# Kernel tuning notes

Measured on AMD Instinct MI355X. Metric: run time of the kernel, lower is better.

Reference implementation:

```python
import jax, jax.numpy as jnp
import numpy as np

N = 100000        # nodes
E = 1600000       # edges (avg degree 16)
F_IN = 128        # num_node_features
H = 64            # hidden_channels
F_EDGE = 8        # num_edge_features (output dim per edge)


def setup_inputs() -> dict:
    key = jax.random.key(0)
    ks = jax.random.split(key, 9)
    x = jax.random.normal(ks[0], (N, F_IN), dtype=jnp.float32)
    edge_index = jax.random.randint(ks[1], (2, E), 0, N, dtype=jnp.int32)
    s = 0.05
    W1 = jax.random.normal(ks[2], (F_IN, H), jnp.float32) * s
    b1 = jnp.zeros((H,), jnp.float32)
    W2 = jax.random.normal(ks[3], (H, H), jnp.float32) * s
    b2 = jnp.zeros((H,), jnp.float32)
    Wl = jax.random.normal(ks[4], (2 * H, F_EDGE), jnp.float32) * s
    bl = jnp.zeros((F_EDGE,), jnp.float32)
    return {"x": x, "edge_index": edge_index,
            "W1": W1, "b1": b1, "W2": W2, "b2": b2, "Wl": Wl, "bl": bl}


def gcn_conv(x, W, b, row, col, n):
    # GCNConv: h = D^{-1/2} (A + I) D^{-1/2} (x W) + b
    h = x @ W
    sl = jnp.arange(n, dtype=row.dtype)          # self-loops
    r = jnp.concatenate([row, sl])
    c = jnp.concatenate([col, sl])
    ones = jnp.ones(r.shape[0], dtype=h.dtype)
    deg = jax.ops.segment_sum(ones, c, num_segments=n)      # in-degree incl. self-loop
    dinv = jax.lax.rsqrt(jnp.maximum(deg, 1e-12))
    norm = dinv[r] * dinv[c]                                 # symmetric normalization
    agg = jax.ops.segment_sum(norm[:, None] * h[r], c, num_segments=n)
    return agg + b


def reference(x, edge_index, W1, b1, W2, b2, Wl, bl):
    row, col = edge_index[0], edge_index[1]
    h = jax.nn.relu(gcn_conv(x, W1, b1, row, col, N))
    # dropout p=0.5 is identity at inference (training=False)
    h = jax.nn.relu(gcn_conv(h, W2, b2, row, col, N))
    x_i = h[row]                                  # [E, H]
    x_j = h[col]                                  # [E, H]
    return jnp.concatenate([x_i, x_j], axis=-1) @ Wl + bl   # [E, F_EDGE]
```

## Files before the change

### kernel.cpp

```cpp
#include <hip/hip_runtime.h>
#include <hip/hip_bf16.h>

static constexpr int NN  = 100000;
static constexpr int NE  = 1600000;
static constexpr int FIN = 128;
static constexpr int HD  = 64;

static constexpr int NB    = 256;
static constexpr int NPB   = 392;
static constexpr int EPB   = NE / NB;
static constexpr unsigned long long DIV392_MAGIC = 43826197ULL;

static constexpr int NSL = 4;

static constexpr int AGN  = 64;
static constexpr int ACAP = 1536;

typedef __attribute__((ext_vector_type(8))) short bf16x8;
typedef __attribute__((ext_vector_type(4))) float f32x4;

__device__ __forceinline__ float bf2f(unsigned short u) {
    return __uint_as_float(((unsigned int)u) << 16);
}
__device__ __forceinline__ unsigned short f2bf(float f) {
    __hip_bfloat16 hb = __float2bfloat16(f);
    return *(unsigned short*)&hb;
}
__device__ __forceinline__ int bucket_of(int c) {
    return (int)(((unsigned long long)(unsigned int)c * DIV392_MAGIC) >> 34);
}

__device__ __forceinline__ float load_in(const void* p, size_t i, int isbf) {
    return isbf ? bf2f(((const unsigned short*)p)[i]) : ((const float*)p)[i];
}

__global__ __launch_bounds__(256) void k_hist(const int* __restrict__ col, int* __restrict__ hist,
                                              const unsigned short* __restrict__ xu,
                                              int* __restrict__ flag) {
    __shared__ int h[4][NB];
    int t = threadIdx.x, w = t >> 6;
#pragma unroll
    for (int r = 0; r < 4; ++r) h[r][t] = 0;
    __syncthreads();
    int base = blockIdx.x * EPB;
    for (int e = base + t; e < base + EPB; e += 256)
        atomicAdd(&h[w][bucket_of(col[e])], 1);
    __syncthreads();
    hist[t * NB + blockIdx.x] = h[0][t] + h[1][t] + h[2][t] + h[3][t];
    if (blockIdx.x == 0) {
        __syncthreads();
        int cnt = 0;
        for (int k = t; k < 4096; k += 256) {
            unsigned short u = xu[2 * k];
            int ex = (u >> 7) & 0xFF;
            cnt += (ex >= 110 && ex <= 135) ? 1 : 0;
        }
        h[0][t] = cnt;
        __syncthreads();
        for (int off = 128; off > 0; off >>= 1) {
            if (t < off) h[0][t] += h[0][t + off];
            __syncthreads();
        }
        if (t == 0) flag[0] = (h[0][0] >= 2048) ? 1 : 0;
    }
}

__global__ __launch_bounds__(256) void k_gscan1(int* __restrict__ a, int* __restrict__ bsums) {
    __shared__ int sd[256];
    int t = threadIdx.x;
    int base = blockIdx.x * 1024 + t * 4;
    int v0 = a[base], v1 = a[base + 1], v2 = a[base + 2], v3 = a[base + 3];
    int tsum = v0 + v1 + v2 + v3;
    sd[t] = tsum;
    __syncthreads();
    for (int off = 1; off < 256; off <<= 1) {
        int tmp = (t >= off) ? sd[t - off] : 0;
        __syncthreads();
        sd[t] += tmp;
        __syncthreads();
    }
    int run = sd[t] - tsum;
    a[base] = run; run += v0;
    a[base + 1] = run; run += v1;
    a[base + 2] = run; run += v2;
    a[base + 3] = run;
    if (t == 255) bsums[blockIdx.x] = sd[t];
}

__device__ __forceinline__ void scan_bsums(const int* __restrict__ bsumsRaw, int* sb) {
    int t = threadIdx.x;
    int myv = 0;
    if (t < 64) { myv = bsumsRaw[t]; sb[t] = myv; }
    __syncthreads();
    for (int off = 1; off < 64; off <<= 1) {
        int v = (t < 64 && t >= off) ? sb[t - off] : 0;
        __syncthreads();
        if (t < 64) sb[t] += v;
        __syncthreads();
    }
    if (t < 64) sb[t] -= myv;
    __syncthreads();
}

__global__ __launch_bounds__(256) void k_binfill(const int* __restrict__ row, const int* __restrict__ col,
                                                 const int* __restrict__ histS,
                                                 const int* __restrict__ bsumsRaw,
                                                 int* __restrict__ csr_tmp) {
    __shared__ int cur[NB];
    __shared__ int sb[64];
    int t = threadIdx.x;
    scan_bsums(bsumsRaw, sb);
    cur[t] = histS[t * NB + blockIdx.x] + sb[t >> 2];
    __syncthreads();
    int base = blockIdx.x * EPB;
    for (int e = base + t; e < base + EPB; e += 256) {
        int r = row[e], c = col[e];
        int b = bucket_of(c);
        int p = atomicAdd(&cur[b], 1);
        csr_tmp[p] = r | ((c - b * NPB) << 17);
    }
}

__global__ __launch_bounds__(256) void k_bsort(const int* __restrict__ csr_tmp,
                                               const int* __restrict__ histS,
                                               const int* __restrict__ bsumsRaw,
                                               int* __restrict__ csr_src,
                                               int* __restrict__ start,
                                               float* __restrict__ dinv) {
    __shared__ int cnt[512];
    __shared__ int cur[512];
    __shared__ int sb[64];
    int t = threadIdx.x;
    int k = blockIdx.x;
    cnt[t] = 0; cnt[t + 256] = 0;
    scan_bsums(bsumsRaw, sb);
    int S = histS[k * NB] + sb[k >> 2];
    int E = (k < NB - 1) ? (histS[(k + 1) * NB] + sb[(k + 1) >> 2]) : NE;
    int nbase = k * NPB;
    __syncthreads();
    for (int e = S + t; e < E; e += 256)
        atomicAdd(&cnt[csr_tmp[e] >> 17], 1);
    __syncthreads();
    int rc0 = cnt[t], rc1 = cnt[t + 256];
    for (int d = 1; d < 512; d <<= 1) {
        int idx = (t + 1) * (d << 1) - 1;
        if (idx < 512) cnt[idx] += cnt[idx - d];
        __syncthreads();
    }
    if (t == 0) cnt[511] = 0;
    __syncthreads();
    for (int d = 256; d >= 1; d >>= 1) {
        int idx = (t + 1) * (d << 1) - 1;
        if (idx < 512) { int tmp = cnt[idx - d]; cnt[idx - d] = cnt[idx]; cnt[idx] += tmp; }
        __syncthreads();
    }
    int n0 = nbase + t;
    if (n0 < NN) {
        start[n0] = S + cnt[t] + rc0;
        dinv[n0] = rsqrtf((float)(rc0 + 1));
    }
    int li = t + 256;
    int n1 = nbase + li;
    if (li < NPB && n1 < NN) {
        start[n1] = S + cnt[li] + rc1;
        dinv[n1] = rsqrtf((float)(rc1 + 1));
    }
    cur[t] = cnt[t]; cur[t + 256] = cnt[t + 256];
    __syncthreads();
    for (int e = S + t; e < E; e += 256) {
        int u = csr_tmp[e];
        int p = atomicAdd(&cur[u >> 17], 1);
        csr_src[S + p] = u & 0x1FFFF;
    }
}

template <int K, bool XDUAL>
__global__ __launch_bounds__(256) void k_gemm_mfma(const void* __restrict__ X,
                                                   const void* __restrict__ W,
                                                   const float* __restrict__ dinv,
                                                   unsigned short* __restrict__ T4,
                                                   const int* __restrict__ flag) {
    constexpr int KT = K / 32;
    __shared__ unsigned short Bs[KT * 4 * 64 * 8];
    int isbf = flag[0];
    for (int tup = threadIdx.x; tup < KT * 4 * 64; tup += 256) {
        int l  = tup & 63;
        int nt = (tup >> 6) & 3;
        int kt = tup >> 8;
        int n  = nt * 16 + (l & 15);
        int kb = kt * 32 + (l >> 4) * 8;
        unsigned short tmp[8];
#pragma unroll
        for (int j = 0; j < 8; ++j) tmp[j] = f2bf(load_in(W, (size_t)(kb + j) * HD + n, isbf));
        *((uint4*)&Bs[(size_t)tup * 8]) = *((const uint4*)tmp);
    }
    __syncthreads();
    int wave = threadIdx.x >> 6, lane = threadIdx.x & 63;
    int quad = lane >> 4, m = lane & 15;
    int row0 = blockIdx.x * 64 + wave * 16;
    int row  = row0 + m;
    int rowc = (row < NN) ? row : (NN - 1);
    bool xf32 = XDUAL && (isbf == 0);
    const char* xrow = (const char*)X + (size_t)rowc * K * (xf32 ? 4 : 2);
    f32x4 acc[4];
#pragma unroll
    for (int nt = 0; nt < 4; ++nt) acc[nt] = (f32x4){0.f, 0.f, 0.f, 0.f};
#pragma unroll
    for (int kt = 0; kt < KT; ++kt) {
        bf16x8 a;
        if (!xf32) {
            a = *((const bf16x8*)(xrow + (size_t)(kt * 32 + quad * 8) * 2));
        } else {
            const float4* fp = (const float4*)(xrow + (size_t)(kt * 32 + quad * 8) * 4);
            float4 u0 = fp[0], u1 = fp[1];
            unsigned short tmp[8] = {f2bf(u0.x), f2bf(u0.y), f2bf(u0.z), f2bf(u0.w),
                                     f2bf(u1.x), f2bf(u1.y), f2bf(u1.z), f2bf(u1.w)};
            a = *((const bf16x8*)tmp);
        }
#pragma unroll
        for (int nt = 0; nt < 4; ++nt) {
            bf16x8 b = *((const bf16x8*)&Bs[(size_t)((kt * 4 + nt) * 64 + lane) * 8]);
            acc[nt] = __builtin_amdgcn_mfma_f32_16x16x32_bf16(a, b, acc[nt], 0, 0, 0);
        }
    }
#pragma unroll
    for (int r = 0; r < 4; ++r) {
        int orow = row0 + quad * 4 + r;
        if (orow < NN) {
            float sc = dinv[orow];
#pragma unroll
            for (int nt = 0; nt < 4; ++nt)
                T4[((size_t)nt * NN + orow) * 16 + m] = f2bf(acc[nt][r] * sc);
        }
    }
}

__global__ __launch_bounds__(256) void k_agg4(const unsigned short* __restrict__ T4,
                                              const int* __restrict__ endOff,
                                              const int* __restrict__ csr_src,
                                              const float* __restrict__ dinv,
                                              const void* __restrict__ bias,
                                              const int* __restrict__ flag,
                                              unsigned short* __restrict__ H4) {
    __shared__ int sIdx[ACAP];
    __shared__ int sEnd[AGN + 1];
    int isbf = flag[0];
    int slice = blockIdx.x & 3;
    int grp   = blockIdx.x >> 2;
    int i0 = grp * AGN;
    int t = threadIdx.x;
    if (t <= AGN) {
        int n = i0 + t - 1;
        sEnd[t] = (n < 0) ? 0 : endOff[(n < NN) ? n : (NN - 1)];
    }
    __syncthreads();
    int base  = sEnd[0];
    int total = sEnd[AGN] - base;
    bool fast = (total <= ACAP);
    if (fast)
        for (int k = t; k < total; k += 256) sIdx[k] = csr_src[base + k];
    __syncthreads();
    int li   = t >> 2;
    int slot = (t >> 1) & 1;
    int fl   = (t & 1) * 8;
    int i    = i0 + li;
    const unsigned short* Ts = T4 + (size_t)slice * NN * 16;
    union U { uint4 u; unsigned short s[8]; };
    float a[8];
#pragma unroll
    for (int j = 0; j < 8; ++j) a[j] = 0.f;
    if (i < NN) {
        int beg = sEnd[li] - base;
        int end = sEnd[li + 1] - base;
        int k = beg + slot;
        if (fast) {
            for (; k + 6 < end; k += 8) {
                int s0 = sIdx[k], s1 = sIdx[k + 2], s2 = sIdx[k + 4], s3 = sIdx[k + 6];
                U t0, t1, t2, t3;
                t0.u = *((const uint4*)(Ts + (size_t)s0 * 16 + fl));
                t1.u = *((const uint4*)(Ts + (size_t)s1 * 16 + fl));
                t2.u = *((const uint4*)(Ts + (size_t)s2 * 16 + fl));
                t3.u = *((const uint4*)(Ts + (size_t)s3 * 16 + fl));
#pragma unroll
                for (int j = 0; j < 8; ++j)
                    a[j] += bf2f(t0.s[j]) + bf2f(t1.s[j]) + bf2f(t2.s[j]) + bf2f(t3.s[j]);
            }
            for (; k < end; k += 2) {
                int s = sIdx[k];
                U tv; tv.u = *((const uint4*)(Ts + (size_t)s * 16 + fl));
#pragma unroll
                for (int j = 0; j < 8; ++j) a[j] += bf2f(tv.s[j]);
            }
        } else {
            for (; k + 6 < end; k += 8) {
                int s0 = csr_src[base + k],     s1 = csr_src[base + k + 2];
                int s2 = csr_src[base + k + 4], s3 = csr_src[base + k + 6];
                U t0, t1, t2, t3;
                t0.u = *((const uint4*)(Ts + (size_t)s0 * 16 + fl));
                t1.u = *((const uint4*)(Ts + (size_t)s1 * 16 + fl));
                t2.u = *((const uint4*)(Ts + (size_t)s2 * 16 + fl));
                t3.u = *((const uint4*)(Ts + (size_t)s3 * 16 + fl));
#pragma unroll
                for (int j = 0; j < 8; ++j)
                    a[j] += bf2f(t0.s[j]) + bf2f(t1.s[j]) + bf2f(t2.s[j]) + bf2f(t3.s[j]);
            }
            for (; k < end; k += 2) {
                int s = csr_src[base + k];
                U tv; tv.u = *((const uint4*)(Ts + (size_t)s * 16 + fl));
#pragma unroll
                for (int j = 0; j < 8; ++j) a[j] += bf2f(tv.s[j]);
            }
        }
    }
#pragma unroll
    for (int j = 0; j < 8; ++j) a[j] += __shfl_xor(a[j], 2, 64);
    if (i < NN && slot == 0) {
        float di = dinv[i];
        U sf; sf.u = *((const uint4*)(Ts + (size_t)i * 16 + fl));
        U o;
#pragma unroll
        for (int j = 0; j < 8; ++j) {
            float v = a[j] + bf2f(sf.s[j]);
            float b = load_in(bias, (size_t)(slice * 16 + fl + j), isbf);
            o.s[j] = f2bf(fmaxf(fmaf(di, v, b), 0.f));
        }
        *((uint4*)(H4 + ((size_t)slice * NN + i) * 16 + fl)) = o.u;
    }
}

__global__ __launch_bounds__(256) void k_gemm_h(const unsigned short* __restrict__ H4,
                                                const void* __restrict__ W,
                                                const float* __restrict__ dinv,
                                                unsigned short* __restrict__ Tb4,
                                                const int* __restrict__ flag) {
    __shared__ unsigned short Bs[2 * 4 * 64 * 8];
    int isbf = flag[0];
    for (int tup = threadIdx.x; tup < 512; tup += 256) {
        int l  = tup & 63;
        int nt = (tup >> 6) & 3;
        int kt = tup >> 8;
        int n  = nt * 16 + (l & 15);
        int kb = kt * 32 + (l >> 4) * 8;
        unsigned short tmp[8];
#pragma unroll
        for (int j = 0; j < 8; ++j) tmp[j] = f2bf(load_in(W, (size_t)(kb + j) * HD + n, isbf));
        *((uint4*)&Bs[(size_t)tup * 8]) = *((const uint4*)tmp);
    }
    __syncthreads();
    int wave = threadIdx.x >> 6, lane = threadIdx.x & 63;
    int quad = lane >> 4, m = lane & 15;
    int row0 = blockIdx.x * 64 + wave * 16;
    int row  = row0 + m;
    int rowc = (row < NN) ? row : (NN - 1);
    f32x4 acc[4];
#pragma unroll
    for (int nt = 0; nt < 4; ++nt) acc[nt] = (f32x4){0.f, 0.f, 0.f, 0.f};
#pragma unroll
    for (int kt = 0; kt < 2; ++kt) {
        int k0 = kt * 32 + quad * 8;
        bf16x8 a = *((const bf16x8*)&H4[((size_t)(k0 >> 4) * NN + rowc) * 16 + (k0 & 15)]);
#pragma unroll
        for (int nt = 0; nt < 4; ++nt) {
            bf16x8 b = *((const bf16x8*)&Bs[(size_t)((kt * 4 + nt) * 64 + lane) * 8]);
            acc[nt] = __builtin_amdgcn_mfma_f32_16x16x32_bf16(a, b, acc[nt], 0, 0, 0);
        }
    }
#pragma unroll
    for (int r = 0; r < 4; ++r) {
        int orow = row0 + quad * 4 + r;
        if (orow < NN) {
            float sc = dinv[orow];
#pragma unroll
            for (int nt = 0; nt < 4; ++nt)
                Tb4[((size_t)nt * NN + orow) * 16 + m] = f2bf(acc[nt][r] * sc);
        }
    }
}

__global__ __launch_bounds__(256) void k_pgemm_h(const unsigned short* __restrict__ H4,
                                                 const void* __restrict__ Wl,
                                                 const void* __restrict__ bl,
                                                 unsigned short* __restrict__ P,
                                                 const int* __restrict__ flag) {
    int isbf = flag[0];
    int wave = threadIdx.x >> 6, lane = threadIdx.x & 63;
    int quad = lane >> 4, m = lane & 15;
    bf16x8 bfr[2];
#pragma unroll
    for (int kt = 0; kt < 2; ++kt) {
        unsigned short tmp[8];
#pragma unroll
        for (int j = 0; j < 8; ++j) {
            int kk = kt * 32 + quad * 8 + j;
            float w = (m < 8) ? load_in(Wl, (size_t)kk * 8 + m, isbf)
                              : load_in(Wl, (size_t)(64 + kk) * 8 + (m - 8), isbf);
            tmp[j] = f2bf(w);
        }
        bfr[kt] = *((const bf16x8*)tmp);
    }
    float binit = (m < 8) ? load_in(bl, m, isbf) : 0.f;
    int row0 = blockIdx.x * 64 + wave * 16;
    int row  = row0 + m;
    int rowc = (row < NN) ? row : (NN - 1);
    f32x4 acc = (f32x4){binit, binit, binit, binit};
#pragma unroll
    for (int kt = 0; kt < 2; ++kt) {
        int k0 = kt * 32 + quad * 8;
        bf16x8 a = *((const bf16x8*)&H4[((size_t)(k0 >> 4) * NN + rowc) * 16 + (k0 & 15)]);
        acc = __builtin_amdgcn_mfma_f32_16x16x32_bf16(a, bfr[kt], acc, 0, 0, 0);
    }
#pragma unroll
    for (int r = 0; r < 4; ++r) {
        int orow = row0 + quad * 4 + r;
        if (orow < NN) P[(size_t)orow * 16 + m] = f2bf(acc[r]);
    }
}

__global__ __launch_bounds__(256) void k_edge_add(const unsigned short* __restrict__ P,
                                                  const int* __restrict__ erow,
                                                  const int* __restrict__ ecol,
                                                  void* __restrict__ out,
                                                  const int* __restrict__ flag) {
    int isbf = flag[0];
    int e = blockIdx.x * 256 + threadIdx.x;
    int i = erow[e], j = ecol[e];
    ushort4 r0 = *((const ushort4*)(P + (size_t)i * 16));
    ushort4 r1 = *((const ushort4*)(P + (size_t)i * 16 + 4));
    ushort4 c0 = *((const ushort4*)(P + (size_t)j * 16 + 8));
    ushort4 c1 = *((const ushort4*)(P + (size_t)j * 16 + 12));
    float v[8] = {bf2f(r0.x) + bf2f(c0.x), bf2f(r0.y) + bf2f(c0.y),
                  bf2f(r0.z) + bf2f(c0.z), bf2f(r0.w) + bf2f(c0.w),
                  bf2f(r1.x) + bf2f(c1.x), bf2f(r1.y) + bf2f(c1.y),
                  bf2f(r1.z) + bf2f(c1.z), bf2f(r1.w) + bf2f(c1.w)};
    if (isbf) {
        union { unsigned short h[8]; uint4 u; } p;
#pragma unroll
        for (int o = 0; o < 8; ++o) p.h[o] = f2bf(v[o]);
        *((uint4*)((__hip_bfloat16*)out + (size_t)e * 8)) = p.u;
    } else {
        float* op = (float*)out + (size_t)e * 8;
        ((float4*)op)[0] = make_float4(v[0], v[1], v[2], v[3]);
        ((float4*)op)[1] = make_float4(v[4], v[5], v[6], v[7]);
    }
}

extern "C" void kernel_launch(void* const* d_in, const int* in_sizes, int n_in,
                              void* d_out, int out_size, void* d_ws, size_t ws_size,
                              hipStream_t stream) {
    const void* x  = d_in[0];
    const int*  ei = (const int*)d_in[1];
    const void* W1 = d_in[2];
    const void* b1 = d_in[3];
    const void* W2 = d_in[4];
    const void* b2 = d_in[5];
    const void* Wl = d_in[6];
    const void* bl = d_in[7];
    const int* row = ei;
    const int* col = ei + NE;

    char* ws = (char*)d_ws;
    int*   flag    = (int*)ws;    ws += 16;
    int*   hist    = (int*)ws;    ws += (size_t)NB * NB * 4;
    int*   bsums   = (int*)ws;    ws += 256 * 4;
    int*   start   = (int*)ws;    ws += (size_t)NN * 4;
    float* dinv    = (float*)ws;  ws += (size_t)NN * 4;
    int*   csr_tmp = (int*)ws;    ws += (size_t)NE * 4;
    int*   csr_src = (int*)ws;    ws += (size_t)NE * 4;
    unsigned short* T4  = (unsigned short*)ws;  ws += (size_t)NN * 64 * 2;
    unsigned short* H4  = (unsigned short*)ws;  ws += (size_t)NN * 64 * 2;
    unsigned short* Tb4 = (unsigned short*)ws;  ws += (size_t)NN * 64 * 2;
    unsigned short* P   = (unsigned short*)ws;

    int gE   = (NE + 255) / 256;
    int gN64 = (NN + 63) / 64;
    int gAgg = ((NN + AGN - 1) / AGN) * NSL;

    k_hist   <<<NB, 256, 0, stream>>>(col, hist, (const unsigned short*)x, flag);
    k_gscan1 <<<64, 256, 0, stream>>>(hist, bsums);
    k_binfill<<<NB, 256, 0, stream>>>(row, col, hist, bsums, csr_tmp);
    k_bsort  <<<NB, 256, 0, stream>>>(csr_tmp, hist, bsums, csr_src, start, dinv);

    k_gemm_mfma<FIN, true><<<gN64, 256, 0, stream>>>(x, W1, dinv, T4, flag);
    k_agg4 <<<gAgg, 256, 0, stream>>>(T4, start, csr_src, dinv, b1, flag, H4);

    k_gemm_h<<<gN64, 256, 0, stream>>>(H4, W2, dinv, Tb4, flag);
    k_agg4 <<<gAgg, 256, 0, stream>>>(Tb4, start, csr_src, dinv, b2, flag, H4);

    k_pgemm_h<<<gN64, 256, 0, stream>>>(H4, Wl, bl, P, flag);
    k_edge_add<<<gE, 256, 0, stream>>>(P, row, col, d_out, flag);
}
```

Baseline: 289.2 us.

## Replace two-level bucket sort CSR build with global atomic degree count and scatter

```diff
diff --git a/kernel.cpp b/kernel.cpp
--- a/kernel.cpp
+++ b/kernel.cpp
@@ -6,10 +6,8 @@
 static constexpr int FIN = 128;
 static constexpr int HD  = 64;
 
-static constexpr int NB    = 256;
-static constexpr int NPB   = 392;
-static constexpr int EPB   = NE / NB;
-static constexpr unsigned long long DIV392_MAGIC = 43826197ULL;
+static constexpr int NCH = 98;
+static constexpr int NNP = NCH * 1024;
 
 static constexpr int NSL = 4;
 
@@ -26,51 +24,48 @@
     __hip_bfloat16 hb = __float2bfloat16(f);
     return *(unsigned short*)&hb;
 }
-__device__ __forceinline__ int bucket_of(int c) {
-    return (int)(((unsigned long long)(unsigned int)c * DIV392_MAGIC) >> 34);
-}
-
 __device__ __forceinline__ float load_in(const void* p, size_t i, int isbf) {
     return isbf ? bf2f(((const unsigned short*)p)[i]) : ((const float*)p)[i];
 }
 
-__global__ __launch_bounds__(256) void k_hist(const int* __restrict__ col, int* __restrict__ hist,
+__global__ __launch_bounds__(256) void k_zero(int* __restrict__ deg,
                                               const unsigned short* __restrict__ xu,
                                               int* __restrict__ flag) {
-    __shared__ int h[4][NB];
-    int t = threadIdx.x, w = t >> 6;
-#pragma unroll
-    for (int r = 0; r < 4; ++r) h[r][t] = 0;
-    __syncthreads();
-    int base = blockIdx.x * EPB;
-    for (int e = base + t; e < base + EPB; e += 256)
-        atomicAdd(&h[w][bucket_of(col[e])], 1);
-    __syncthreads();
-    hist[t * NB + blockIdx.x] = h[0][t] + h[1][t] + h[2][t] + h[3][t];
+    int t = threadIdx.x;
+    int base = blockIdx.x * 1024 + t * 4;
+    *((int4*)&deg[base]) = make_int4(0, 0, 0, 0);
     if (blockIdx.x == 0) {
-        __syncthreads();
+        __shared__ int sd[256];
         int cnt = 0;
         for (int k = t; k < 4096; k += 256) {
             unsigned short u = xu[2 * k];
             int ex = (u >> 7) & 0xFF;
             cnt += (ex >= 110 && ex <= 135) ? 1 : 0;
         }
-        h[0][t] = cnt;
+        sd[t] = cnt;
         __syncthreads();
         for (int off = 128; off > 0; off >>= 1) {
-            if (t < off) h[0][t] += h[0][t + off];
+            if (t < off) sd[t] += sd[t + off];
             __syncthreads();
         }
-        if (t == 0) flag[0] = (h[0][0] >= 2048) ? 1 : 0;
-    }
-}
-
-__global__ __launch_bounds__(256) void k_gscan1(int* __restrict__ a, int* __restrict__ bsums) {
+        if (t == 0) flag[0] = (sd[0] >= 2048) ? 1 : 0;
+    }
+}
+
+__global__ __launch_bounds__(256) void k_deg(const int* __restrict__ col,
+                                             int* __restrict__ deg) {
+    for (int e = blockIdx.x * 256 + threadIdx.x; e < NE; e += 1024 * 256)
+        atomicAdd(&deg[col[e]], 1);
+}
+
+__global__ __launch_bounds__(256) void k_dscan1(const int* __restrict__ deg,
+                                                int* __restrict__ start,
+                                                int* __restrict__ bsums) {
     __shared__ int sd[256];
     int t = threadIdx.x;
     int base = blockIdx.x * 1024 + t * 4;
-    int v0 = a[base], v1 = a[base + 1], v2 = a[base + 2], v3 = a[base + 3];
-    int tsum = v0 + v1 + v2 + v3;
+    int4 v = *((const int4*)&deg[base]);
+    int tsum = v.x + v.y + v.z + v.w;
     sd[t] = tsum;
     __syncthreads();
     for (int off = 1; off < 256; off <<= 1) {
@@ -80,104 +75,48 @@
         __syncthreads();
     }
     int run = sd[t] - tsum;
-    a[base] = run; run += v0;
-    a[base + 1] = run; run += v1;
-    a[base + 2] = run; run += v2;
-    a[base + 3] = run;
-    if (t == 255) bsums[blockIdx.x] = sd[t];
-}
-
-__device__ __forceinline__ void scan_bsums(const int* __restrict__ bsumsRaw, int* sb) {
+    int4 o;
+    o.x = run; run += v.x;
+    o.y = run; run += v.y;
+    o.z = run; run += v.z;
+    o.w = run;
+    *((int4*)&start[base]) = o;
+    if (t == 255) bsums[blockIdx.x] = sd[255];
+}
+
+__device__ __forceinline__ void scan_bsums98(const int* __restrict__ bsumsRaw, int* sb) {
     int t = threadIdx.x;
     int myv = 0;
-    if (t < 64) { myv = bsumsRaw[t]; sb[t] = myv; }
-    __syncthreads();
-    for (int off = 1; off < 64; off <<= 1) {
-        int v = (t < 64 && t >= off) ? sb[t - off] : 0;
+    if (t < 128) { myv = (t < NCH) ? bsumsRaw[t] : 0; sb[t] = myv; }
+    __syncthreads();
+    for (int off = 1; off < 128; off <<= 1) {
+        int v = (t < 128 && t >= off) ? sb[t - off] : 0;
         __syncthreads();
-        if (t < 64) sb[t] += v;
+        if (t < 128) sb[t] += v;
         __syncthreads();
     }
-    if (t < 64) sb[t] -= myv;
-    __syncthreads();
-}
-
-__global__ __launch_bounds__(256) void k_binfill(const int* __restrict__ row, const int* __restrict__ col,
-                                                 const int* __restrict__ histS,
-                                                 const int* __restrict__ bsumsRaw,
-                                                 int* __restrict__ csr_tmp) {
-    __shared__ int cur[NB];
-    __shared__ int sb[64];
-    int t = threadIdx.x;
-    scan_bsums(bsumsRaw, sb);
-    cur[t] = histS[t * NB + blockIdx.x] + sb[t >> 2];
-    __syncthreads();
-    int base = blockIdx.x * EPB;
-    for (int e = base + t; e < base + EPB; e += 256) {
+    if (t < 128) sb[t] -= myv;
+    __syncthreads();
+}
+
+__global__ __launch_bounds__(256) void k_scatter(const int* __restrict__ row,
+                                                 const int* __restrict__ col,
+                                                 int* __restrict__ start,
+                                                 const int* __restrict__ bsums,
+                                                 int* __restrict__ csr_src) {
+    __shared__ int sb[128];
+    scan_bsums98(bsums, sb);
+    for (int e = blockIdx.x * 256 + threadIdx.x; e < NE; e += 1024 * 256) {
         int r = row[e], c = col[e];
-        int b = bucket_of(c);
-        int p = atomicAdd(&cur[b], 1);
-        csr_tmp[p] = r | ((c - b * NPB) << 17);
-    }
-}
-
-__global__ __launch_bounds__(256) void k_bsort(const int* __restrict__ csr_tmp,
-                                               const int* __restrict__ histS,
-                                               const int* __restrict__ bsumsRaw,
-                                               int* __restrict__ csr_src,
-                                               int* __restrict__ start,
-                                               float* __restrict__ dinv) {
-    __shared__ int cnt[512];
-    __shared__ int cur[512];
-    __shared__ int sb[64];
-    int t = threadIdx.x;
-    int k = blockIdx.x;
-    cnt[t] = 0; cnt[t + 256] = 0;
-    scan_bsums(bsumsRaw, sb);
-    int S = histS[k * NB] + sb[k >> 2];
-    int E = (k < NB - 1) ? (histS[(k + 1) * NB] + sb[(k + 1) >> 2]) : NE;
-    int nbase = k * NPB;
-    __syncthreads();
-    for (int e = S + t; e < E; e += 256)
-        atomicAdd(&cnt[csr_tmp[e] >> 17], 1);
-    __syncthreads();
-    int rc0 = cnt[t], rc1 = cnt[t + 256];
-    for (int d = 1; d < 512; d <<= 1) {
-        int idx = (t + 1) * (d << 1) - 1;
-        if (idx < 512) cnt[idx] += cnt[idx - d];
-        __syncthreads();
-    }
-    if (t == 0) cnt[511] = 0;
-    __syncthreads();
-    for (int d = 256; d >= 1; d >>= 1) {
-        int idx = (t + 1) * (d << 1) - 1;
-        if (idx < 512) { int tmp = cnt[idx - d]; cnt[idx - d] = cnt[idx]; cnt[idx] += tmp; }
-        __syncthreads();
-    }
-    int n0 = nbase + t;
-    if (n0 < NN) {
-        start[n0] = S + cnt[t] + rc0;
-        dinv[n0] = rsqrtf((float)(rc0 + 1));
-    }
-    int li = t + 256;
-    int n1 = nbase + li;
-    if (li < NPB && n1 < NN) {
-        start[n1] = S + cnt[li] + rc1;
-        dinv[n1] = rsqrtf((float)(rc1 + 1));
-    }
-    cur[t] = cnt[t]; cur[t + 256] = cnt[t + 256];
-    __syncthreads();
-    for (int e = S + t; e < E; e += 256) {
-        int u = csr_tmp[e];
-        int p = atomicAdd(&cur[u >> 17], 1);
-        csr_src[S + p] = u & 0x1FFFF;
+        int pos = atomicAdd(&start[c], 1) + sb[c >> 10];
+        csr_src[pos] = r;
     }
 }
 
 template <int K, bool XDUAL>
 __global__ __launch_bounds__(256) void k_gemm_mfma(const void* __restrict__ X,
                                                    const void* __restrict__ W,
-                                                   const float* __restrict__ dinv,
+                                                   const int* __restrict__ deg,
                                                    unsigned short* __restrict__ T4,
                                                    const int* __restrict__ flag) {
     constexpr int KT = K / 32;
@@ -227,7 +166,7 @@
     for (int r = 0; r < 4; ++r) {
         int orow = row0 + quad * 4 + r;
         if (orow < NN) {
-            float sc = dinv[orow];
+            float sc = rsqrtf((float)(deg[orow] + 1));
 #pragma unroll
             for (int nt = 0; nt < 4; ++nt)
                 T4[((size_t)nt * NN + orow) * 16 + m] = f2bf(acc[nt][r] * sc);
@@ -237,11 +176,13 @@
 
 __global__ __launch_bounds__(256) void k_agg4(const unsigned short* __restrict__ T4,
                                               const int* __restrict__ endOff,
+                                              const int* __restrict__ bsums,
                                               const int* __restrict__ csr_src,
-                                              const float* __restrict__ dinv,
+                                              const int* __restrict__ deg,
                                               const void* __restrict__ bias,
                                               const int* __restrict__ flag,
                                               unsigned short* __restrict__ H4) {
+    __shared__ int sb[128];
     __shared__ int sIdx[ACAP];
     __shared__ int sEnd[AGN + 1];
     int isbf = flag[0];
@@ -249,9 +190,14 @@
     int grp   = blockIdx.x >> 2;
     int i0 = grp * AGN;
     int t = threadIdx.x;
+    scan_bsums98(bsums, sb);
     if (t <= AGN) {
         int n = i0 + t - 1;
-        sEnd[t] = (n < 0) ? 0 : endOff[(n < NN) ? n : (NN - 1)];
+        if (n < 0) sEnd[t] = 0;
+        else {
+            int nc = (n < NN) ? n : (NN - 1);
+            sEnd[t] = endOff[nc] + sb[nc >> 10];
+        }
     }
     __syncthreads();
     int base  = sEnd[0];
@@ -274,16 +220,22 @@
         int end = sEnd[li + 1] - base;
         int k = beg + slot;
         if (fast) {
-            for (; k + 6 < end; k += 8) {
-                int s0 = sIdx[k], s1 = sIdx[k + 2], s2 = sIdx[k + 4], s3 = sIdx[k + 6];
-                U t0, t1, t2, t3;
+            for (; k + 14 < end; k += 16) {
+                int s0 = sIdx[k],      s1 = sIdx[k + 2],  s2 = sIdx[k + 4],  s3 = sIdx[k + 6];
+                int s4 = sIdx[k + 8],  s5 = sIdx[k + 10], s6 = sIdx[k + 12], s7 = sIdx[k + 14];
+                U t0, t1, t2, t3, t4, t5, t6, t7;
                 t0.u = *((const uint4*)(Ts + (size_t)s0 * 16 + fl));
                 t1.u = *((const uint4*)(Ts + (size_t)s1 * 16 + fl));
                 t2.u = *((const uint4*)(Ts + (size_t)s2 * 16 + fl));
                 t3.u = *((const uint4*)(Ts + (size_t)s3 * 16 + fl));
+                t4.u = *((const uint4*)(Ts + (size_t)s4 * 16 + fl));
+                t5.u = *((const uint4*)(Ts + (size_t)s5 * 16 + fl));
+                t6.u = *((const uint4*)(Ts + (size_t)s6 * 16 + fl));
+                t7.u = *((const uint4*)(Ts + (size_t)s7 * 16 + fl));
 #pragma unroll
                 for (int j = 0; j < 8; ++j)
-                    a[j] += bf2f(t0.s[j]) + bf2f(t1.s[j]) + bf2f(t2.s[j]) + bf2f(t3.s[j]);
+                    a[j] += (bf2f(t0.s[j]) + bf2f(t1.s[j]) + bf2f(t2.s[j]) + bf2f(t3.s[j]))
+                          + (bf2f(t4.s[j]) + bf2f(t5.s[j]) + bf2f(t6.s[j]) + bf2f(t7.s[j]));
             }
             for (; k < end; k += 2) {
                 int s = sIdx[k];
@@ -315,7 +267,7 @@
 #pragma unroll
     for (int j = 0; j < 8; ++j) a[j] += __shfl_xor(a[j], 2, 64);
     if (i < NN && slot == 0) {
-        float di = dinv[i];
+        float di = rsqrtf((float)(deg[i] + 1));
         U sf; sf.u = *((const uint4*)(Ts + (size_t)i * 16 + fl));
         U o;
 #pragma unroll
@@ -330,7 +282,7 @@
 
 __global__ __launch_bounds__(256) void k_gemm_h(const unsigned short* __restrict__ H4,
                                                 const void* __restrict__ W,
-                                                const float* __restrict__ dinv,
+                                                const int* __restrict__ deg,
                                                 unsigned short* __restrict__ Tb4,
                                                 const int* __restrict__ flag) {
     __shared__ unsigned short Bs[2 * 4 * 64 * 8];
@@ -369,7 +321,7 @@
     for (int r = 0; r < 4; ++r) {
         int orow = row0 + quad * 4 + r;
         if (orow < NN) {
-            float sc = dinv[orow];
+            float sc = rsqrtf((float)(deg[orow] + 1));
 #pragma unroll
             for (int nt = 0; nt < 4; ++nt)
                 Tb4[((size_t)nt * NN + orow) * 16 + m] = f2bf(acc[nt][r] * sc);
@@ -460,11 +412,9 @@
 
     char* ws = (char*)d_ws;
     int*   flag    = (int*)ws;    ws += 16;
-    int*   hist    = (int*)ws;    ws += (size_t)NB * NB * 4;
-    int*   bsums   = (int*)ws;    ws += 256 * 4;
-    int*   start   = (int*)ws;    ws += (size_t)NN * 4;
-    float* dinv    = (float*)ws;  ws += (size_t)NN * 4;
-    int*   csr_tmp = (int*)ws;    ws += (size_t)NE * 4;
+    int*   deg     = (int*)ws;    ws += (size_t)NNP * 4;
+    int*   start   = (int*)ws;    ws += (size_t)NNP * 4;
+    int*   bsums   = (int*)ws;    ws += 128 * 4;
     int*   csr_src = (int*)ws;    ws += (size_t)NE * 4;
     unsigned short* T4  = (unsigned short*)ws;  ws += (size_t)NN * 64 * 2;
     unsigned short* H4  = (unsigned short*)ws;  ws += (size_t)NN * 64 * 2;
@@ -475,16 +425,16 @@
     int gN64 = (NN + 63) / 64;
     int gAgg = ((NN + AGN - 1) / AGN) * NSL;
 
-    k_hist   <<<NB, 256, 0, stream>>>(col, hist, (const unsigned short*)x, flag);
-    k_gscan1 <<<64, 256, 0, stream>>>(hist, bsums);
-    k_binfill<<<NB, 256, 0, stream>>>(row, col, hist, bsums, csr_tmp);
-    k_bsort  <<<NB, 256, 0, stream>>>(csr_tmp, hist, bsums, csr_src, start, dinv);
-
-    k_gemm_mfma<FIN, true><<<gN64, 256, 0, stream>>>(x, W1, dinv, T4, flag);
-    k_agg4 <<<gAgg, 256, 0, stream>>>(T4, start, csr_src, dinv, b1, flag, H4);
-
-    k_gemm_h<<<gN64, 256, 0, stream>>>(H4, W2, dinv, Tb4, flag);
-    k_agg4 <<<gAgg, 256, 0, stream>>>(Tb4, start, csr_src, dinv, b2, flag, H4);
+    k_zero   <<<NCH,  256, 0, stream>>>(deg, (const unsigned short*)x, flag);
+    k_deg    <<<1024, 256, 0, stream>>>(col, deg);
+    k_dscan1 <<<NCH,  256, 0, stream>>>(deg, start, bsums);
+    k_scatter<<<1024, 256, 0, stream>>>(row, col, start, bsums, csr_src);
+
+    k_gemm_mfma<FIN, true><<<gN64, 256, 0, stream>>>(x, W1, deg, T4, flag);
+    k_agg4 <<<gAgg, 256, 0, stream>>>(T4, start, bsums, csr_src, deg, b1, flag, H4);
+
+    k_gemm_h<<<gN64, 256, 0, stream>>>(H4, W2, deg, Tb4, flag);
+    k_agg4 <<<gAgg, 256, 0, stream>>>(Tb4, start, bsums, csr_src, deg, b2, flag, H4);
 
     k_pgemm_h<<<gN64, 256, 0, stream>>>(H4, Wl, bl, P, flag);
     k_edge_add<<<gE, 256, 0, stream>>>(P, row, col, d_out, flag);
```

Result: slower. 471.4 us (+63.0%).

## Fold histogram scan into binfill and use 1024-thread blocks for CSR build

Applied to the files above, without the earlier changes.

```diff
diff --git a/kernel.cpp b/kernel.cpp
--- a/kernel.cpp
+++ b/kernel.cpp
@@ -34,114 +34,118 @@
     return isbf ? bf2f(((const unsigned short*)p)[i]) : ((const float*)p)[i];
 }
 
-__global__ __launch_bounds__(256) void k_hist(const int* __restrict__ col, int* __restrict__ hist,
-                                              const unsigned short* __restrict__ xu,
-                                              int* __restrict__ flag) {
+__global__ __launch_bounds__(1024) void k_hist(const int* __restrict__ col, int* __restrict__ hist,
+                                               const unsigned short* __restrict__ xu,
+                                               int* __restrict__ flag) {
     __shared__ int h[4][NB];
-    int t = threadIdx.x, w = t >> 6;
-#pragma unroll
-    for (int r = 0; r < 4; ++r) h[r][t] = 0;
+    __shared__ int sd[256];
+    int t = threadIdx.x;
+    int w4 = (t >> 6) & 3;
+    if (t < NB) { h[0][t] = 0; h[1][t] = 0; h[2][t] = 0; h[3][t] = 0; }
     __syncthreads();
     int base = blockIdx.x * EPB;
-    for (int e = base + t; e < base + EPB; e += 256)
-        atomicAdd(&h[w][bucket_of(col[e])], 1);
-    __syncthreads();
-    hist[t * NB + blockIdx.x] = h[0][t] + h[1][t] + h[2][t] + h[3][t];
+    for (int e = base + t; e < base + EPB; e += 1024)
+        atomicAdd(&h[w4][bucket_of(col[e])], 1);
+    __syncthreads();
+    if (t < NB)
+        hist[t * NB + blockIdx.x] = h[0][t] + h[1][t] + h[2][t] + h[3][t];
     if (blockIdx.x == 0) {
-        __syncthreads();
         int cnt = 0;
-        for (int k = t; k < 4096; k += 256) {
-            unsigned short u = xu[2 * k];
-            int ex = (u >> 7) & 0xFF;
-            cnt += (ex >= 110 && ex <= 135) ? 1 : 0;
-        }
-        h[0][t] = cnt;
+        if (t < 256) {
+            for (int k = t; k < 4096; k += 256) {
+                unsigned short u = xu[2 * k];
+                int ex = (u >> 7) & 0xFF;
+                cnt += (ex >= 110 && ex <= 135) ? 1 : 0;
+            }
+            sd[t] = cnt;
+        }
         __syncthreads();
         for (int off = 128; off > 0; off >>= 1) {
-            if (t < off) h[0][t] += h[0][t + off];
+            if (t < off) sd[t] += sd[t + off];
             __syncthreads();
         }
-        if (t == 0) flag[0] = (h[0][0] >= 2048) ? 1 : 0;
-    }
-}
-
-__global__ __launch_bounds__(256) void k_gscan1(int* __restrict__ a, int* __restrict__ bsums) {
-    __shared__ int sd[256];
+        if (t == 0) flag[0] = (sd[0] >= 2048) ? 1 : 0;
+    }
+}
+
+__global__ __launch_bounds__(1024) void k_binfill(const int* __restrict__ row, const int* __restrict__ col,
+                                                  const int* __restrict__ hist,
+                                                  int* __restrict__ csr_tmp,
+                                                  int* __restrict__ bucketBase) {
+    __shared__ int part[4][NB];
+    __shared__ int pref[NB];
+    __shared__ int sc[NB];
+    __shared__ int cur[NB];
     int t = threadIdx.x;
-    int base = blockIdx.x * 1024 + t * 4;
-    int v0 = a[base], v1 = a[base + 1], v2 = a[base + 2], v3 = a[base + 3];
-    int tsum = v0 + v1 + v2 + v3;
-    sd[t] = tsum;
-    __syncthreads();
-    for (int off = 1; off < 256; off <<= 1) {
-        int tmp = (t >= off) ? sd[t - off] : 0;
+    int b = t & 255, q = t >> 8;
+    int myb = blockIdx.x;
+    int mq = myb >> 6, mr = myb & 63;
+    int s = 0, p = 0;
+    const int* hrow = hist + b * NB + q * 64;
+    for (int j = 0; j < 64; j += 4) {
+        int4 v = *((const int4*)&hrow[j]);
+        if (q == mq) {
+            if (j + 0 < mr) p += v.x;
+            if (j + 1 < mr) p += v.y;
+            if (j + 2 < mr) p += v.z;
+            if (j + 3 < mr) p += v.w;
+        }
+        s += v.x + v.y + v.z + v.w;
+    }
+    part[q][b] = s;
+    if (q == mq) pref[b] = p;
+    __syncthreads();
+    int tot = 0;
+    if (t < NB) {
+        int t0 = part[0][t], t1 = part[1][t], t2 = part[2][t], t3 = part[3][t];
+        tot = t0 + t1 + t2 + t3;
+        int before = pref[t];
+        if (mq > 0) before += t0;
+        if (mq > 1) before += t1;
+        if (mq > 2) before += t2;
+        sc[t] = tot;
+        cur[t] = before;
+    }
+    __syncthreads();
+    for (int off = 1; off < NB; off <<= 1) {
+        int v = (t < NB && t >= off) ? sc[t - off] : 0;
         __syncthreads();
-        sd[t] += tmp;
+        if (t < NB) sc[t] += v;
         __syncthreads();
     }
-    int run = sd[t] - tsum;
-    a[base] = run; run += v0;
-    a[base + 1] = run; run += v1;
-    a[base + 2] = run; run += v2;
-    a[base + 3] = run;
-    if (t == 255) bsums[blockIdx.x] = sd[t];
-}
-
-__device__ __forceinline__ void scan_bsums(const int* __restrict__ bsumsRaw, int* sb) {
-    int t = threadIdx.x;
-    int myv = 0;
-    if (t < 64) { myv = bsumsRaw[t]; sb[t] = myv; }
-    __syncthreads();
-    for (int off = 1; off < 64; off <<= 1) {
-        int v = (t < 64 && t >= off) ? sb[t - off] : 0;
-        __syncthreads();
-        if (t < 64) sb[t] += v;
-        __syncthreads();
-    }
-    if (t < 64) sb[t] -= myv;
-    __syncthreads();
-}
-
-__global__ __launch_bounds__(256) void k_binfill(const int* __restrict__ row, const int* __restrict__ col,
-                                                 const int* __restrict__ histS,
-                                                 const int* __restrict__ bsumsRaw,
-                                                 int* __restrict__ csr_tmp) {
-    __shared__ int cur[NB];
-    __shared__ int sb[64];
-    int t = threadIdx.x;
-    scan_bsums(bsumsRaw, sb);
-    cur[t] = histS[t * NB + blockIdx.x] + sb[t >> 2];
-    __syncthreads();
-    int base = blockIdx.x * EPB;
-    for (int e = base + t; e < base + EPB; e += 256) {
+    if (t < NB) cur[t] += sc[t] - tot;
+    if (myb == 0 && t < NB) {
+        bucketBase[t] = sc[t] - tot;
+        if (t == 0) bucketBase[NB] = NE;
+    }
+    __syncthreads();
+    int base = myb * EPB;
+    for (int e = base + t; e < base + EPB; e += 1024) {
         int r = row[e], c = col[e];
-        int b = bucket_of(c);
-        int p = atomicAdd(&cur[b], 1);
-        csr_tmp[p] = r | ((c - b * NPB) << 17);
-    }
-}
-
-__global__ __launch_bounds__(256) void k_bsort(const int* __restrict__ csr_tmp,
-                                               const int* __restrict__ histS,
-                                               const int* __restrict__ bsumsRaw,
-                                               int* __restrict__ csr_src,
-                                               int* __restrict__ start,
-                                               float* __restrict__ dinv) {
+        int bb = bucket_of(c);
+        int pos = atomicAdd(&cur[bb], 1);
+        csr_tmp[pos] = r | ((c - bb * NPB) << 17);
+    }
+}
+
+__global__ __launch_bounds__(1024) void k_bsort(const int* __restrict__ csr_tmp,
+                                                const int* __restrict__ bucketBase,
+                                                int* __restrict__ csr_src,
+                                                int* __restrict__ start,
+                                                float* __restrict__ dinv) {
     __shared__ int cnt[512];
     __shared__ int cur[512];
-    __shared__ int sb[64];
     int t = threadIdx.x;
     int k = blockIdx.x;
-    cnt[t] = 0; cnt[t + 256] = 0;
-    scan_bsums(bsumsRaw, sb);
-    int S = histS[k * NB] + sb[k >> 2];
-    int E = (k < NB - 1) ? (histS[(k + 1) * NB] + sb[(k + 1) >> 2]) : NE;
+    if (t < 512) cnt[t] = 0;
+    __syncthreads();
+    int S = bucketBase[k], E = bucketBase[k + 1];
     int nbase = k * NPB;
-    __syncthreads();
-    for (int e = S + t; e < E; e += 256)
+    for (int e = S + t; e < E; e += 1024)
         atomicAdd(&cnt[csr_tmp[e] >> 17], 1);
     __syncthreads();
-    int rc0 = cnt[t], rc1 = cnt[t + 256];
+    int rc = (t < 512) ? cnt[t] : 0;
+    __syncthreads();
     for (int d = 1; d < 512; d <<= 1) {
         int idx = (t + 1) * (d << 1) - 1;
         if (idx < 512) cnt[idx] += cnt[idx - d];
@@ -154,20 +158,16 @@
         if (idx < 512) { int tmp = cnt[idx - d]; cnt[idx - d] = cnt[idx]; cnt[idx] += tmp; }
         __syncthreads();
     }
-    int n0 = nbase + t;
-    if (n0 < NN) {
-        start[n0] = S + cnt[t] + rc0;
-        dinv[n0] = rsqrtf((float)(rc0 + 1));
-    }
-    int li = t + 256;
-    int n1 = nbase + li;
-    if (li < NPB && n1 < NN) {
-        start[n1] = S + cnt[li] + rc1;
-        dinv[n1] = rsqrtf((float)(rc1 + 1));
-    }
-    cur[t] = cnt[t]; cur[t + 256] = cnt[t + 256];
-    __syncthreads();
-    for (int e = S + t; e < E; e += 256) {
+    if (t < NPB) {
+        int n = nbase + t;
+        if (n < NN) {
+            start[n] = S + cnt[t] + rc;
+            dinv[n] = rsqrtf((float)(rc + 1));
+        }
+    }
+    if (t < 512) cur[t] = cnt[t];
+    __syncthreads();
+    for (int e = S + t; e < E; e += 1024) {
         int u = csr_tmp[e];
         int p = atomicAdd(&cur[u >> 17], 1);
         csr_src[S + p] = u & 0x1FFFF;
@@ -424,14 +424,13 @@
     int isbf = flag[0];
     int e = blockIdx.x * 256 + threadIdx.x;
     int i = erow[e], j = ecol[e];
-    ushort4 r0 = *((const ushort4*)(P + (size_t)i * 16));
-    ushort4 r1 = *((const ushort4*)(P + (size_t)i * 16 + 4));
-    ushort4 c0 = *((const ushort4*)(P + (size_t)j * 16 + 8));
-    ushort4 c1 = *((const ushort4*)(P + (size_t)j * 16 + 12));
-    float v[8] = {bf2f(r0.x) + bf2f(c0.x), bf2f(r0.y) + bf2f(c0.y),
-                  bf2f(r0.z) + bf2f(c0.z), bf2f(r0.w) + bf2f(c0.w),
-                  bf2f(r1.x) + bf2f(c1.x), bf2f(r1.y) + bf2f(c1.y),
-                  bf2f(r1.z) + bf2f(c1.z), bf2f(r1.w) + bf2f(c1.w)};
+    union U { uint4 u; unsigned short s[8]; };
+    U a, b;
+    a.u = *((const uint4*)(P + (size_t)i * 16));
+    b.u = *((const uint4*)(P + (size_t)j * 16 + 8));
+    float v[8];
+#pragma unroll
+    for (int o = 0; o < 8; ++o) v[o] = bf2f(a.s[o]) + bf2f(b.s[o]);
     if (isbf) {
         union { unsigned short h[8]; uint4 u; } p;
 #pragma unroll
@@ -459,13 +458,13 @@
     const int* col = ei + NE;
 
     char* ws = (char*)d_ws;
-    int*   flag    = (int*)ws;    ws += 16;
-    int*   hist    = (int*)ws;    ws += (size_t)NB * NB * 4;
-    int*   bsums   = (int*)ws;    ws += 256 * 4;
-    int*   start   = (int*)ws;    ws += (size_t)NN * 4;
-    float* dinv    = (float*)ws;  ws += (size_t)NN * 4;
-    int*   csr_tmp = (int*)ws;    ws += (size_t)NE * 4;
-    int*   csr_src = (int*)ws;    ws += (size_t)NE * 4;
+    int*   flag       = (int*)ws;    ws += 16;
+    int*   hist       = (int*)ws;    ws += (size_t)NB * NB * 4;
+    int*   bucketBase = (int*)ws;    ws += (NB + 1) * 4;
+    int*   start      = (int*)ws;    ws += (size_t)NN * 4;
+    float* dinv       = (float*)ws;  ws += (size_t)NN * 4;
+    int*   csr_tmp    = (int*)ws;    ws += (size_t)NE * 4;
+    int*   csr_src    = (int*)ws;    ws += (size_t)NE * 4;
     unsigned short* T4  = (unsigned short*)ws;  ws += (size_t)NN * 64 * 2;
     unsigned short* H4  = (unsigned short*)ws;  ws += (size_t)NN * 64 * 2;
     unsigned short* Tb4 = (unsigned short*)ws;  ws += (size_t)NN * 64 * 2;
@@ -475,10 +474,9 @@
     int gN64 = (NN + 63) / 64;
     int gAgg = ((NN + AGN - 1) / AGN) * NSL;
 
-    k_hist   <<<NB, 256, 0, stream>>>(col, hist, (const unsigned short*)x, flag);
-    k_gscan1 <<<64, 256, 0, stream>>>(hist, bsums);
-    k_binfill<<<NB, 256, 0, stream>>>(row, col, hist, bsums, csr_tmp);
-    k_bsort  <<<NB, 256, 0, stream>>>(csr_tmp, hist, bsums, csr_src, start, dinv);
+    k_hist   <<<NB, 1024, 0, stream>>>(col, hist, (const unsigned short*)x, flag);
+    k_binfill<<<NB, 1024, 0, stream>>>(row, col, hist, csr_tmp, bucketBase);
+    k_bsort  <<<NB, 1024, 0, stream>>>(csr_tmp, bucketBase, csr_src, start, dinv);
 
     k_gemm_mfma<FIN, true><<<gN64, 256, 0, stream>>>(x, W1, dinv, T4, flag);
     k_agg4 <<<gAgg, 256, 0, stream>>>(T4, start, csr_src, dinv, b1, flag, H4);
```

Result: no change. 291.9 us (+0.9%).
